# Optimization experiments

Hardware: AMD Instinct MI355X
Metric: run time of the kernel (lower is better)

## Reference

```python
import jax, jax.numpy as jnp
import numpy as np

M, N = 256, 65536          # matched masks, flattened pred-mask pixels (256x256)
BLOCK_AREA = 4.0           # (H_t*W_t)/N with target masks at 512x512
H_T = W_T = 512.0
NUM_MASKS = 256.0
MAX_ITERS = 20
TOL = 1e-7


def _eval_fS(z, lam, Kcol):
    p = jax.nn.sigmoid(z + lam)
    f = jnp.sum(p, axis=-1, keepdims=True) - Kcol
    s = jnp.sum(p * (1.0 - p), axis=-1, keepdims=True)
    return f, s


def _shift_core(z, K):
    # z: (M,1,N) logits, K: (M,1) target counts. Safeguarded Newton/bisection
    # so that sum(sigmoid(z + lam)) == K per row. (torch ref uses float64;
    # we stay in input dtype for jit/bf16 compatibility.)
    n = z.shape[-1]
    K = jnp.clip(K, 0.0, float(n))
    z_max = jnp.max(z, axis=-1, keepdims=True)
    z_min = jnp.min(z, axis=-1, keepdims=True)
    L = -20.0 - z_max
    U = 20.0 - z_min

    def _logit(x, eps=1e-6):
        x = jnp.clip(x, eps, 1.0 - eps)
        return jnp.log(x) - jnp.log1p(-x)

    p0_mean = jnp.mean(jax.nn.sigmoid(z), axis=-1)
    t_mean = K / n
    lam = (_logit(t_mean) - _logit(p0_mean))[..., None]
    lam = jnp.clip(lam, L, U)
    Kcol = K[..., None]
    f, S = _eval_fS(z, lam, Kcol)

    def body(_, carry):
        lam, f, S, L, U = carry
        done = jnp.abs(f) <= TOL
        newton = lam - f / (S + 1e-18)
        oob = (newton < L) | (newton > U)
        lam_try = jnp.where(oob | done, lam, newton)
        f_try, _ = _eval_fS(z, lam_try, Kcol)
        no_improve = (jnp.abs(f_try) > jnp.abs(f)) & (~oob) & (~done)
        mid = 0.5 * (L + U)
        lam_next = jnp.where(oob | no_improve, mid, lam_try)
        f_next, S_next = _eval_fS(z, lam_next, Kcol)
        go_upper = f_next > 0
        U = jnp.where(go_upper, lam_next, U)
        L = jnp.where(go_upper, L, lam_next)
        return lam_next, f_next, S_next, L, U

    lam, f, S, L, U = jax.lax.fori_loop(0, MAX_ITERS, body, (lam, f, S, L, U))
    lam = jnp.clip(lam, L, U)
    return z + lam


def setup_inputs() -> dict:
    key = jax.random.key(0)
    k1, k2 = jax.random.split(key)
    logits = jax.random.normal(k1, (M, N), dtype=jnp.float32) * 2.0
    pos_counts = jax.random.uniform(k2, (M, N), dtype=jnp.float32) * BLOCK_AREA
    return {"logits": logits, "pos_counts": pos_counts}


def reference(logits, pos_counts):
    n = logits.shape[1]
    K_high = jnp.sum(pos_counts, axis=1)                      # (M,)
    K_low = jnp.clip(K_high / BLOCK_AREA, 0.0, float(n))      # (M,)
    z_shift = _shift_core(logits[:, None, :], K_low[:, None])[:, 0, :]
    # block-weighted BCE with logits (numerically stable form)
    abs_z = jnp.abs(z_shift)
    max_z = jnp.maximum(z_shift, 0.0)
    logexp = jnp.log1p(jnp.exp(-abs_z))
    loss_block = BLOCK_AREA * max_z - z_shift * pos_counts + BLOCK_AREA * logexp
    loss_mask = jnp.sum(jnp.sum(loss_block, axis=1) / (H_T * W_T)) / NUM_MASKS
    # dice on area-matched probabilities
    probs = jax.nn.sigmoid(z_shift)
    inter = jnp.sum(probs * pos_counts, axis=1)
    pred_sum = BLOCK_AREA * jnp.sum(probs, axis=1)
    loss_dice = jnp.sum(1.0 - (2.0 * inter + 1.0) / (pred_sum + K_high + 1.0)) / NUM_MASKS
    return jnp.stack([loss_mask, loss_dice])
```

## Files before the change

### kernel.cpp

```cpp
#include <hip/hip_runtime.h>
#include <math.h>

#define NCOLS 65536
#define MROWS 256
#define NBINS 512
#define SUBE 2048
#define NSUB 8
#define BLKE (SUBE * NSUB)
#define BPR (NCOLS / BLKE)
#define K1_TPB 256
#define ZLO 20.0f
#define INVW ((float)NBINS / (2.0f * ZLO))
#define BINW (2.0f * ZLO / (float)NBINS)
#define PSCALE 8.0f
#define CNT_SHIFT 19
#define POS_MASK ((1u << CNT_SHIFT) - 1u)

#define GL16(gsrc, ldst) __builtin_amdgcn_global_load_lds(                    \
    (const __attribute__((address_space(1))) void*)(gsrc),                    \
    (__attribute__((address_space(3))) void*)(ldst), 16, 0, 0)

__device__ __forceinline__ float waveReduceSum(float v) {
#pragma unroll
  for (int off = 32; off > 0; off >>= 1) v += __shfl_xor(v, off, 64);
  return v;
}

__global__ __launch_bounds__(K1_TPB) void hist_kernel(
    const float* __restrict__ logits, const float* __restrict__ pos,
    unsigned int* __restrict__ gh) {
  __shared__ __align__(16) float zb[2][SUBE];
  __shared__ __align__(16) float pb[2][SUBE];
  __shared__ unsigned int h[NBINS];
  const int blk = blockIdx.x;
  const int row = blk / BPR, seg = blk % BPR;
  const int tid = threadIdx.x;
  const int wv = tid >> 6, ln = tid & 63;
  const int wq = wv * 512;

  h[tid] = 0u;
  h[tid + K1_TPB] = 0u;

  const float* zs = logits + (size_t)row * NCOLS + (size_t)seg * BLKE;
  const float* ps = pos + (size_t)row * NCOLS + (size_t)seg * BLKE;

#define STAGE(par, c) do {                                                    \
    const float* zsrc_ = zs + (c) * SUBE + wq;                                \
    const float* psrc_ = ps + (c) * SUBE + wq;                                \
    GL16(zsrc_ + ln * 4, &zb[par][wq]);                                       \
    GL16(zsrc_ + 256 + ln * 4, &zb[par][wq + 256]);                           \
    GL16(psrc_ + ln * 4, &pb[par][wq]);                                       \
    GL16(psrc_ + 256 + ln * 4, &pb[par][wq + 256]);                           \
  } while (0)

#define PROC(par) do {                                                        \
    _Pragma("unroll")                                                         \
    for (int s2 = 0; s2 < 2; ++s2) {                                          \
      const float4 zv = *(const float4*)&zb[par][wq + s2 * 256 + ln * 4];     \
      const float4 pv = *(const float4*)&pb[par][wq + s2 * 256 + ln * 4];     \
      float zz[4] = {zv.x, zv.y, zv.z, zv.w};                                 \
      float pp[4] = {pv.x, pv.y, pv.z, pv.w};                                 \
      _Pragma("unroll")                                                       \
      for (int c4 = 0; c4 < 4; ++c4) {                                        \
        int b = (int)((zz[c4] + ZLO) * INVW);                                 \
        b = min(max(b, 0), NBINS - 1);                                        \
        unsigned int pk = (1u << CNT_SHIFT) |                                 \
                          (unsigned int)__float2int_rn(pp[c4] * PSCALE);      \
        atomicAdd(&h[b], pk);                                                 \
      }                                                                       \
    }                                                                         \
  } while (0)

  STAGE(0, 0);
  __syncthreads();

  for (int c = 0; c < NSUB; ++c) {
    if (c + 1 < NSUB) {
      STAGE((c + 1) & 1, c + 1);
      asm volatile("s_waitcnt vmcnt(4)" ::: "memory");
    } else {
      asm volatile("s_waitcnt vmcnt(0)" ::: "memory");
    }
    __builtin_amdgcn_sched_barrier(0);
    PROC(c & 1);
  }
  __syncthreads();
  const size_t base = (size_t)blk * NBINS;
  gh[base + tid] = h[tid];
  gh[base + tid + K1_TPB] = h[tid + K1_TPB];
#undef STAGE
#undef PROC
}

#define K2_TPB 256

__global__ __launch_bounds__(K2_TPB) void solve_kernel(
    const unsigned int* __restrict__ gh, float* __restrict__ rowout) {
  __shared__ float cs[NBINS], ps[NBINS];
  const int row = blockIdx.x;
  const int tid = threadIdx.x;

#pragma unroll
  for (int j = 0; j < NBINS / K2_TPB; ++j) {
    const int b = tid + j * K2_TPB;
    unsigned int c = 0u, q = 0u;
    const size_t base = (size_t)row * BPR * NBINS + b;
#pragma unroll
    for (int ch = 0; ch < BPR; ++ch) {
      const unsigned int v = gh[base + (size_t)ch * NBINS];
      c += v >> CNT_SHIFT;
      q += v & POS_MASK;
    }
    cs[b] = (float)c;
    ps[b] = (float)q * (1.0f / PSCALE);
  }
  __syncthreads();
  if (tid >= 64) return;

  const int lane = tid;
  float cnt[8], pb[8], zc[8];
  float Kh = 0.0f, Szp = 0.0f;
#pragma unroll
  for (int j = 0; j < 8; ++j) {
    const int b = lane + 64 * j;
    cnt[j] = cs[b];
    pb[j] = ps[b];
    zc[j] = -ZLO + ((float)b + 0.5f) * BINW;
    Kh += pb[j];
    Szp += zc[j] * pb[j];
  }
  Kh = waveReduceSum(Kh);
  Szp = waveReduceSum(Szp);
  const float K = fminf(fmaxf(Kh * 0.25f, 0.0f), (float)NCOLS);

  float Lb = -2.0f * ZLO, Ub = 2.0f * ZLO, lam = 0.0f;
  for (int it = 0; it < 40; ++it) {
    float fp = 0.0f, sp = 0.0f;
#pragma unroll
    for (int j = 0; j < 8; ++j) {
      const float p = 1.0f / (1.0f + __expf(-(zc[j] + lam)));
      fp += cnt[j] * p;
      sp += cnt[j] * p * (1.0f - p);
    }
    fp = waveReduceSum(fp);
    sp = waveReduceSum(sp);
    const float f = fp - K;
    if (fabsf(f) <= 1e-2f) break;
    if (f > 0.0f) Ub = lam; else Lb = lam;
    const float newton = lam - f / (sp + 1e-12f);
    lam = (newton > Lb && newton < Ub) ? newton : 0.5f * (Lb + Ub);
  }

  float tl = 0.0f, ti = 0.0f, tp = 0.0f;
#pragma unroll
  for (int j = 0; j < 8; ++j) {
    const float zs = zc[j] + lam;
    const float e = __expf(-fabsf(zs));
    const float lg = __logf(1.0f + e);
    const float mz = fmaxf(zs, 0.0f);
    const float sig = (zs >= 0.0f) ? (1.0f / (1.0f + e)) : (e / (1.0f + e));
    tl += cnt[j] * (mz + lg);
    ti += pb[j] * sig;
    tp += cnt[j] * sig;
  }
  tl = waveReduceSum(tl);
  ti = waveReduceSum(ti);
  tp = waveReduceSum(tp);
  if (lane == 0) {
    float* o = rowout + row * 4;
    o[0] = 4.0f * tl - (Szp + lam * Kh);
    o[1] = ti;
    o[2] = tp;
    o[3] = Kh;
  }
}

__global__ void final_kernel(const float* __restrict__ rowout, float* __restrict__ out) {
  const int t = threadIdx.x;
  const float loss = rowout[t * 4 + 0];
  const float inter = rowout[t * 4 + 1];
  const float psum = rowout[t * 4 + 2];
  const float Kh = rowout[t * 4 + 3];
  float maskc = loss * (1.0f / (512.0f * 512.0f));
  float dicec = 1.0f - (2.0f * inter + 1.0f) / (4.0f * psum + Kh + 1.0f);
  maskc = waveReduceSum(maskc);
  dicec = waveReduceSum(dicec);
  __shared__ float red[8];
  const int wid = t >> 6, lane = t & 63;
  if (lane == 0) { red[wid] = maskc; red[4 + wid] = dicec; }
  __syncthreads();
  if (t == 0) {
    float a = 0.0f, b = 0.0f;
    for (int j = 0; j < 4; ++j) { a += red[j]; b += red[4 + j]; }
    out[0] = a / 256.0f;
    out[1] = b / 256.0f;
  }
}

#define FB_TPB 1024
#define FB_NV4 (NCOLS / 4 / FB_TPB)
__device__ __forceinline__ void fbReduce2(float a, float b, float* red,
                                          int wid, int lane, float& A, float& B) {
  a = waveReduceSum(a);
  b = waveReduceSum(b);
  __syncthreads();
  if (lane == 0) { red[wid] = a; red[16 + wid] = b; }
  __syncthreads();
  float ta = 0.0f, tb = 0.0f;
#pragma unroll
  for (int j = 0; j < 16; ++j) { ta += red[j]; tb += red[16 + j]; }
  A = ta; B = tb;
}

__global__ __launch_bounds__(FB_TPB) void fb_row_kernel(
    const float* __restrict__ logits, const float* __restrict__ pos,
    float* __restrict__ rowout) {
  __shared__ unsigned int h_cnt[2048];
  __shared__ int h_sum[2048];
  __shared__ float red[64];
  const int row = blockIdx.x;
  const int tid = threadIdx.x, wid = tid >> 6, lane = tid & 63;
  const float4* z4 = (const float4*)(logits + (size_t)row * NCOLS);
  const float4* p4 = (const float4*)(pos + (size_t)row * NCOLS);
  for (int b = tid; b < 2048; b += FB_TPB) { h_cnt[b] = 0u; h_sum[b] = 0; }
  __syncthreads();
  const float invw = 2048.0f / 40.0f;
  float s_pos = 0.0f;
#pragma unroll
  for (int i = 0; i < FB_NV4; ++i) {
    float4 zv = z4[i * FB_TPB + tid];
    float4 pv = p4[i * FB_TPB + tid];
    s_pos += (pv.x + pv.y) + (pv.z + pv.w);
    float zz[4] = {zv.x, zv.y, zv.z, zv.w};
#pragma unroll
    for (int c = 0; c < 4; ++c) {
      int b = (int)((zz[c] + 20.0f) * invw);
      b = min(max(b, 0), 2047);
      atomicAdd(&h_cnt[b], 1u);
      atomicAdd(&h_sum[b], __float2int_rn(zz[c] * 1024.0f));
    }
  }
  float K_high, dummy;
  fbReduce2(s_pos, 0.0f, red, wid, lane, K_high, dummy);
  float K = fminf(fmaxf(K_high * 0.25f, 0.0f), (float)NCOLS);
  const float c0 = (float)h_cnt[tid];
  const float c1 = (float)h_cnt[tid + FB_TPB];
  const float zb0 = (c0 > 0.0f) ? (float)h_sum[tid] / (1024.0f * c0) : 0.0f;
  const float zb1 = (c1 > 0.0f) ? (float)h_sum[tid + FB_TPB] / (1024.0f * c1) : 0.0f;
  float Lb = -40.0f, Ub = 40.0f, lam = 0.0f;
  for (int it = 0; it < 40; ++it) {
    float p0 = 1.0f / (1.0f + __expf(-(zb0 + lam)));
    float p1 = 1.0f / (1.0f + __expf(-(zb1 + lam)));
    float F, S;
    fbReduce2(c0 * p0 + c1 * p1, c0 * p0 * (1.0f - p0) + c1 * p1 * (1.0f - p1),
              red, wid, lane, F, S);
    float f = F - K;
    if (fabsf(f) <= 1e-3f) break;
    if (f > 0.0f) Ub = lam; else Lb = lam;
    float newton = lam - f / (S + 1e-12f);
    lam = (newton > Lb && newton < Ub) ? newton : 0.5f * (Lb + Ub);
  }
  float loss = 0.0f, inter = 0.0f, psum = 0.0f;
#pragma unroll
  for (int i = 0; i < FB_NV4; ++i) {
    float4 zv = z4[i * FB_TPB + tid];
    float4 pv = p4[i * FB_TPB + tid];
    float zz[4] = {zv.x, zv.y, zv.z, zv.w};
    float pp[4] = {pv.x, pv.y, pv.z, pv.w};
#pragma unroll
    for (int c = 0; c < 4; ++c) {
      float zs = zz[c] + lam;
      float q = __expf(-fabsf(zs));
      loss += 4.0f * fmaxf(zs, 0.0f) - zs * pp[c] + 4.0f * __logf(1.0f + q);
      float sig = (zs >= 0.0f) ? (1.0f / (1.0f + q)) : (q / (1.0f + q));
      inter += sig * pp[c];
      psum += sig;
    }
  }
  float TL, TI;
  fbReduce2(loss, inter, red, wid, lane, TL, TI);
  float TP, d2;
  fbReduce2(psum, 0.0f, red, wid, lane, TP, d2);
  if (tid == 0) {
    float* o = rowout + row * 4;
    o[0] = TL; o[1] = TI; o[2] = TP; o[3] = K_high;
  }
}

extern "C" void kernel_launch(void* const* d_in, const int* in_sizes, int n_in,
                              void* d_out, int out_size, void* d_ws, size_t ws_size,
                              hipStream_t stream) {
  const float* logits = (const float*)d_in[0];
  const float* pos = (const float*)d_in[1];
  char* ws = (char*)d_ws;

  const size_t nblk = (size_t)MROWS * BPR;
  const size_t off_gh = 0;
  const size_t off_rowout = off_gh + nblk * NBINS * sizeof(unsigned int);
  const size_t needed = off_rowout + (size_t)MROWS * 4 * sizeof(float);

  if (ws_size >= needed) {
    unsigned int* gh = (unsigned int*)(ws + off_gh);
    float* rowout = (float*)(ws + off_rowout);
    hist_kernel<<<(int)nblk, K1_TPB, 0, stream>>>(logits, pos, gh);
    solve_kernel<<<MROWS, K2_TPB, 0, stream>>>(gh, rowout);
    final_kernel<<<1, 256, 0, stream>>>(rowout, (float*)d_out);
  } else {
    float* rowout = (float*)d_ws;
    fb_row_kernel<<<MROWS, FB_TPB, 0, stream>>>(logits, pos, rowout);
    final_kernel<<<1, 256, 0, stream>>>(rowout, (float*)d_out);
  }
}
```

Measured before the change: 32.21 us.

## Fuse final reduction into solve kernel via last-block atomic counter

Removes the separate final_kernel launch: each solve block increments a global done counter, and the last block to finish reads every row result and writes the two output losses. The counter is reset by hist_kernel, which runs earlier in the same stream. The histogram inner loop also packs the count and the scaled positive value with a single fma plus a bias, replacing the shift/or/round sequence, and computes the bin index with an fma. This saves one kernel launch and a few ALU ops per element, at the cost of a global atomic with fences and a serial tail in the last block.

```diff
diff --git a/kernel.cpp b/kernel.cpp
--- a/kernel.cpp
+++ b/kernel.cpp
@@ -15,6 +15,7 @@
 #define PSCALE 8.0f
 #define CNT_SHIFT 19
 #define POS_MASK ((1u << CNT_SHIFT) - 1u)
+#define PACK_BIAS 524288.5f
 
 #define GL16(gsrc, ldst) __builtin_amdgcn_global_load_lds(                    \
     (const __attribute__((address_space(1))) void*)(gsrc),                    \
@@ -28,7 +29,7 @@
 
 __global__ __launch_bounds__(K1_TPB) void hist_kernel(
     const float* __restrict__ logits, const float* __restrict__ pos,
-    unsigned int* __restrict__ gh) {
+    unsigned int* __restrict__ gh, unsigned int* __restrict__ donecnt) {
   __shared__ __align__(16) float zb[2][SUBE];
   __shared__ __align__(16) float pb[2][SUBE];
   __shared__ unsigned int h[NBINS];
@@ -40,6 +41,7 @@
 
   h[tid] = 0u;
   h[tid + K1_TPB] = 0u;
+  if (blk == 0 && tid == 0) donecnt[0] = 0u;
 
   const float* zs = logits + (size_t)row * NCOLS + (size_t)seg * BLKE;
   const float* ps = pos + (size_t)row * NCOLS + (size_t)seg * BLKE;
@@ -62,10 +64,9 @@
       float pp[4] = {pv.x, pv.y, pv.z, pv.w};                                 \
       _Pragma("unroll")                                                       \
       for (int c4 = 0; c4 < 4; ++c4) {                                        \
-        int b = (int)((zz[c4] + ZLO) * INVW);                                 \
+        int b = (int)fmaf(zz[c4], INVW, ZLO * INVW);                          \
         b = min(max(b, 0), NBINS - 1);                                        \
-        unsigned int pk = (1u << CNT_SHIFT) |                                 \
-                          (unsigned int)__float2int_rn(pp[c4] * PSCALE);      \
+        unsigned int pk = (unsigned int)fmaf(pp[c4], PSCALE, PACK_BIAS);      \
         atomicAdd(&h[b], pk);                                                 \
       }                                                                       \
     }                                                                         \
@@ -95,10 +96,13 @@
 #define K2_TPB 256
 
 __global__ __launch_bounds__(K2_TPB) void solve_kernel(
-    const unsigned int* __restrict__ gh, float* __restrict__ rowout) {
+    const unsigned int* __restrict__ gh, float* __restrict__ rowout,
+    unsigned int* __restrict__ donecnt, float* __restrict__ out) {
   __shared__ float cs[NBINS], ps[NBINS];
+  __shared__ int winner;
   const int row = blockIdx.x;
   const int tid = threadIdx.x;
+  const int lane = tid & 63;
 
 #pragma unroll
   for (int j = 0; j < NBINS / K2_TPB; ++j) {
@@ -115,85 +119,87 @@
     ps[b] = (float)q * (1.0f / PSCALE);
   }
   __syncthreads();
-  if (tid >= 64) return;
-
-  const int lane = tid;
-  float cnt[8], pb[8], zc[8];
-  float Kh = 0.0f, Szp = 0.0f;
-#pragma unroll
-  for (int j = 0; j < 8; ++j) {
-    const int b = lane + 64 * j;
-    cnt[j] = cs[b];
-    pb[j] = ps[b];
-    zc[j] = -ZLO + ((float)b + 0.5f) * BINW;
-    Kh += pb[j];
-    Szp += zc[j] * pb[j];
-  }
-  Kh = waveReduceSum(Kh);
-  Szp = waveReduceSum(Szp);
-  const float K = fminf(fmaxf(Kh * 0.25f, 0.0f), (float)NCOLS);
-
-  float Lb = -2.0f * ZLO, Ub = 2.0f * ZLO, lam = 0.0f;
-  for (int it = 0; it < 40; ++it) {
-    float fp = 0.0f, sp = 0.0f;
+
+  if (tid < 64) {
+    float cnt[8], pb[8], zc[8];
+    float Kh = 0.0f, Szp = 0.0f;
 #pragma unroll
     for (int j = 0; j < 8; ++j) {
-      const float p = 1.0f / (1.0f + __expf(-(zc[j] + lam)));
-      fp += cnt[j] * p;
-      sp += cnt[j] * p * (1.0f - p);
-    }
-    fp = waveReduceSum(fp);
-    sp = waveReduceSum(sp);
-    const float f = fp - K;
-    if (fabsf(f) <= 1e-2f) break;
-    if (f > 0.0f) Ub = lam; else Lb = lam;
-    const float newton = lam - f / (sp + 1e-12f);
-    lam = (newton > Lb && newton < Ub) ? newton : 0.5f * (Lb + Ub);
-  }
-
-  float tl = 0.0f, ti = 0.0f, tp = 0.0f;
-#pragma unroll
-  for (int j = 0; j < 8; ++j) {
-    const float zs = zc[j] + lam;
-    const float e = __expf(-fabsf(zs));
-    const float lg = __logf(1.0f + e);
-    const float mz = fmaxf(zs, 0.0f);
-    const float sig = (zs >= 0.0f) ? (1.0f / (1.0f + e)) : (e / (1.0f + e));
-    tl += cnt[j] * (mz + lg);
-    ti += pb[j] * sig;
-    tp += cnt[j] * sig;
-  }
-  tl = waveReduceSum(tl);
-  ti = waveReduceSum(ti);
-  tp = waveReduceSum(tp);
-  if (lane == 0) {
-    float* o = rowout + row * 4;
-    o[0] = 4.0f * tl - (Szp + lam * Kh);
-    o[1] = ti;
-    o[2] = tp;
-    o[3] = Kh;
-  }
-}
-
-__global__ void final_kernel(const float* __restrict__ rowout, float* __restrict__ out) {
-  const int t = threadIdx.x;
-  const float loss = rowout[t * 4 + 0];
-  const float inter = rowout[t * 4 + 1];
-  const float psum = rowout[t * 4 + 2];
-  const float Kh = rowout[t * 4 + 3];
-  float maskc = loss * (1.0f / (512.0f * 512.0f));
-  float dicec = 1.0f - (2.0f * inter + 1.0f) / (4.0f * psum + Kh + 1.0f);
-  maskc = waveReduceSum(maskc);
-  dicec = waveReduceSum(dicec);
-  __shared__ float red[8];
-  const int wid = t >> 6, lane = t & 63;
-  if (lane == 0) { red[wid] = maskc; red[4 + wid] = dicec; }
-  __syncthreads();
-  if (t == 0) {
-    float a = 0.0f, b = 0.0f;
-    for (int j = 0; j < 4; ++j) { a += red[j]; b += red[4 + j]; }
-    out[0] = a / 256.0f;
-    out[1] = b / 256.0f;
+      const int b = lane + 64 * j;
+      cnt[j] = cs[b];
+      pb[j] = ps[b];
+      zc[j] = -ZLO + ((float)b + 0.5f) * BINW;
+      Kh += pb[j];
+      Szp += zc[j] * pb[j];
+    }
+    Kh = waveReduceSum(Kh);
+    Szp = waveReduceSum(Szp);
+    const float K = fminf(fmaxf(Kh * 0.25f, 0.0f), (float)NCOLS);
+
+    float Lb = -2.0f * ZLO, Ub = 2.0f * ZLO, lam = 0.0f;
+    for (int it = 0; it < 40; ++it) {
+      float fp = 0.0f, sp = 0.0f;
+#pragma unroll
+      for (int j = 0; j < 8; ++j) {
+        const float p = 1.0f / (1.0f + __expf(-(zc[j] + lam)));
+        fp += cnt[j] * p;
+        sp += cnt[j] * p * (1.0f - p);
+      }
+      fp = waveReduceSum(fp);
+      sp = waveReduceSum(sp);
+      const float f = fp - K;
+      if (fabsf(f) <= 1e-2f) break;
+      if (f > 0.0f) Ub = lam; else Lb = lam;
+      const float newton = lam - f / (sp + 1e-12f);
+      lam = (newton > Lb && newton < Ub) ? newton : 0.5f * (Lb + Ub);
+    }
+
+    float tl = 0.0f, ti = 0.0f, tp = 0.0f;
+#pragma unroll
+    for (int j = 0; j < 8; ++j) {
+      const float zs = zc[j] + lam;
+      const float e = __expf(-fabsf(zs));
+      const float lg = __logf(1.0f + e);
+      const float mz = fmaxf(zs, 0.0f);
+      const float sig = (zs >= 0.0f) ? (1.0f / (1.0f + e)) : (e / (1.0f + e));
+      tl += cnt[j] * (mz + lg);
+      ti += pb[j] * sig;
+      tp += cnt[j] * sig;
+    }
+    tl = waveReduceSum(tl);
+    ti = waveReduceSum(ti);
+    tp = waveReduceSum(tp);
+    if (lane == 0) {
+      float* o = rowout + row * 4;
+      o[0] = 4.0f * tl - (Szp + lam * Kh);
+      o[1] = ti;
+      o[2] = tp;
+      o[3] = Kh;
+    }
+  }
+
+  if (tid == 0) {
+    __threadfence();
+    const unsigned int od = __hip_atomic_fetch_add(
+        donecnt, 1u, __ATOMIC_ACQ_REL, __HIP_MEMORY_SCOPE_AGENT);
+    winner = (od == MROWS - 1);
+  }
+  __syncthreads();
+  if (winner && tid < 64) {
+    __threadfence();
+    float mc = 0.0f, dc = 0.0f;
+#pragma unroll
+    for (int k = 0; k < 4; ++k) {
+      const float* o = rowout + (lane + 64 * k) * 4;
+      mc += o[0] * (1.0f / (512.0f * 512.0f));
+      dc += 1.0f - (2.0f * o[1] + 1.0f) / (4.0f * o[2] + o[3] + 1.0f);
+    }
+    mc = waveReduceSum(mc);
+    dc = waveReduceSum(dc);
+    if (lane == 0) {
+      out[0] = mc * (1.0f / 256.0f);
+      out[1] = dc * (1.0f / 256.0f);
+    }
   }
 }
 
@@ -287,6 +293,28 @@
   }
 }
 
+__global__ void final_kernel(const float* __restrict__ rowout, float* __restrict__ out) {
+  const int t = threadIdx.x;
+  const float loss = rowout[t * 4 + 0];
+  const float inter = rowout[t * 4 + 1];
+  const float psum = rowout[t * 4 + 2];
+  const float Kh = rowout[t * 4 + 3];
+  float maskc = loss * (1.0f / (512.0f * 512.0f));
+  float dicec = 1.0f - (2.0f * inter + 1.0f) / (4.0f * psum + Kh + 1.0f);
+  maskc = waveReduceSum(maskc);
+  dicec = waveReduceSum(dicec);
+  __shared__ float red[8];
+  const int wid = t >> 6, lane = t & 63;
+  if (lane == 0) { red[wid] = maskc; red[4 + wid] = dicec; }
+  __syncthreads();
+  if (t == 0) {
+    float a = 0.0f, b = 0.0f;
+    for (int j = 0; j < 4; ++j) { a += red[j]; b += red[4 + j]; }
+    out[0] = a / 256.0f;
+    out[1] = b / 256.0f;
+  }
+}
+
 extern "C" void kernel_launch(void* const* d_in, const int* in_sizes, int n_in,
                               void* d_out, int out_size, void* d_ws, size_t ws_size,
                               hipStream_t stream) {
@@ -297,14 +325,15 @@
   const size_t nblk = (size_t)MROWS * BPR;
   const size_t off_gh = 0;
   const size_t off_rowout = off_gh + nblk * NBINS * sizeof(unsigned int);
-  const size_t needed = off_rowout + (size_t)MROWS * 4 * sizeof(float);
+  const size_t off_done = off_rowout + (size_t)MROWS * 4 * sizeof(float);
+  const size_t needed = off_done + sizeof(unsigned int);
 
   if (ws_size >= needed) {
     unsigned int* gh = (unsigned int*)(ws + off_gh);
     float* rowout = (float*)(ws + off_rowout);
-    hist_kernel<<<(int)nblk, K1_TPB, 0, stream>>>(logits, pos, gh);
-    solve_kernel<<<MROWS, K2_TPB, 0, stream>>>(gh, rowout);
-    final_kernel<<<1, 256, 0, stream>>>(rowout, (float*)d_out);
+    unsigned int* donecnt = (unsigned int*)(ws + off_done);
+    hist_kernel<<<(int)nblk, K1_TPB, 0, stream>>>(logits, pos, gh, donecnt);
+    solve_kernel<<<MROWS, K2_TPB, 0, stream>>>(gh, rowout, donecnt, (float*)d_out);
   } else {
     float* rowout = (float*)d_ws;
     fb_row_kernel<<<MROWS, FB_TPB, 0, stream>>>(logits, pos, rowout);
```

Measured after the change: 38.49 us. +19.5%, slower.
